# Kernel optimization log

Measured on AMD Instinct MI355X. Metric: run time of the kernel, lower is better.

Reference implementation:

```python
import jax, jax.numpy as jnp
import numpy as np

N, E = 50000, 800000
DN, DE, H = 128, 64, 8
C = DN // H  # per-head dim = 16


def setup_inputs() -> dict:
    key = jax.random.key(0)
    ks = jax.random.split(key, 16)
    s = 0.05
    inp = {
        "node_state": jax.random.normal(ks[0], (N, DN), jnp.float32),
        "edge_index": jax.random.randint(ks[1], (2, E), 0, N, jnp.int64 if jax.config.jax_enable_x64 else jnp.int32),
        "edge_state": jax.random.normal(ks[2], (E, DE), jnp.float32),
        # edge_proj: Linear(DE, DE)
        "W_edge": jax.random.normal(ks[3], (DE, DE), jnp.float32) * s,
        "b_edge": jnp.zeros((DE,), jnp.float32),
        # TransformerConv linears (in, out) layout: y = x @ W + b
        "Wq": jax.random.normal(ks[4], (DN, DN), jnp.float32) * s,
        "bq": jnp.zeros((DN,), jnp.float32),
        "Wk": jax.random.normal(ks[5], (DN, DN), jnp.float32) * s,
        "bk": jnp.zeros((DN,), jnp.float32),
        "Wv": jax.random.normal(ks[6], (DN, DN), jnp.float32) * s,
        "bv": jnp.zeros((DN,), jnp.float32),
        "We": jax.random.normal(ks[7], (DE, DN), jnp.float32) * s,  # lin_edge, no bias
        "Wskip": jax.random.normal(ks[8], (DN, DN), jnp.float32) * s,
        "bskip": jnp.zeros((DN,), jnp.float32),
        "Wbeta": jax.random.normal(ks[9], (3 * DN, 1), jnp.float32) * s,  # lin_beta, no bias
        "ln_g": jnp.ones((DN,), jnp.float32),
        "ln_b": jnp.zeros((DN,), jnp.float32),
    }
    return inp


def reference(node_state, edge_index, edge_state, W_edge, b_edge, Wq, bq, Wk, bk,
              Wv, bv, We, Wskip, bskip, Wbeta, ln_g, ln_b):
    n = node_state.shape[0]
    src, dst = edge_index[0], edge_index[1]

    # edge_proj
    edge_attr = edge_state @ W_edge + b_edge  # [E, DE]

    # TransformerConv (beta=True, concat=True, dropout in eval mode)
    q = (node_state @ Wq + bq).reshape(n, H, C)
    k = (node_state @ Wk + bk).reshape(n, H, C)
    v = (node_state @ Wv + bv).reshape(n, H, C)
    e = (edge_attr @ We).reshape(-1, H, C)  # [E, H, C]

    kj = k[src] + e                                        # [E, H, C]
    alpha = jnp.sum(q[dst] * kj, axis=-1) / np.sqrt(C)     # [E, H]

    # segment softmax over destination nodes
    amax = jax.ops.segment_max(alpha, dst, num_segments=n)  # [N, H]
    ex = jnp.exp(alpha - amax[dst])
    denom = jax.ops.segment_sum(ex, dst, num_segments=n)    # [N, H]
    a = ex / denom[dst]                                     # [E, H]

    msg = (v[src] + e) * a[:, :, None]                      # [E, H, C]
    out = jax.ops.segment_sum(msg, dst, num_segments=n).reshape(n, DN)

    # beta-gated skip
    x_r = node_state @ Wskip + bskip
    beta = jax.nn.sigmoid(jnp.concatenate([out, x_r, out - x_r], axis=-1) @ Wbeta)  # [N, 1]
    out = beta * x_r + (1.0 - beta) * out

    # LayerNorm
    mu = jnp.mean(out, axis=-1, keepdims=True)
    var = jnp.mean(jnp.square(out - mu), axis=-1, keepdims=True)
    normed = (out - mu) * jax.lax.rsqrt(var + 1e-5) * ln_g + ln_b

    # residual + relu (dropout is identity in eval)
    return node_state + jax.nn.relu(normed)
```

## Files before the change

kernel.cpp:

```cpp
#include <hip/hip_runtime.h>
#include <cstdint>
#include <cstddef>

#define NN 50000
#define NE 800000

typedef short bf16x8 __attribute__((ext_vector_type(8)));
typedef float f32x4 __attribute__((ext_vector_type(4)));
typedef float f32x2 __attribute__((ext_vector_type(2)));

__device__ __forceinline__ float b2f(unsigned short s) {
  union { unsigned int u; float f; } x; x.u = ((unsigned int)s) << 16; return x.f;
}
__device__ __forceinline__ unsigned short f2b(float f) {
  union { float f; unsigned int u; } x; x.f = f;
  unsigned int r = x.u + 0x7FFFu + ((x.u >> 16) & 1u);
  return (unsigned short)(r >> 16);
}

#define WS_WCE    0u
#define WS_BCE    16384u
#define WS_WCEF   20480u
#define WS_WALLF  40960u
#define WS_BALL   172032u
#define WS_QB     180224u
#define WS_KB     12980224u
#define WS_VB     25780224u
#define WS_XR     38580224u
#define WS_EB     64180224u
#define WS_CNT    268980224u
#define WS_OFF    269180224u
#define WS_CUR    269380224u
#define WS_BSUM   269580224u
#define WS_POS    269584320u
#define WS_SRCS   272784320u

__global__ void k_prep(const float* __restrict__ W_edge, const float* __restrict__ b_edge,
                       const float* __restrict__ We, unsigned short* __restrict__ wce,
                       float* __restrict__ bce) {
  int i = blockIdx.x;
  int j = threadIdx.x;
  float s = 0.f;
  for (int m = 0; m < 64; ++m) s += W_edge[i*64+m] * We[m*128+j];
  wce[i*128+j] = f2b(s);
  if (i == 0) {
    float bb = 0.f;
    for (int m = 0; m < 64; ++m) bb += b_edge[m] * We[m*128+j];
    bce[j] = bb;
  }
}

__global__ void k_pack_wce(const unsigned short* __restrict__ wce, unsigned short* __restrict__ wcef) {
  int fb = blockIdx.x;
  int ct = fb >> 1, s = fb & 1;
  int l = threadIdx.x;
  unsigned short* dst = wcef + (((size_t)(ct*2+s))*64 + l)*8;
  int col = ct*16 + (l & 15);
  int k0 = s*32 + (l >> 4)*8;
  #pragma unroll
  for (int j = 0; j < 8; ++j) dst[j] = wce[(k0+j)*128 + col];
}

__global__ void k_pack_wall(const float* __restrict__ Wq, const float* __restrict__ Wk,
                            const float* __restrict__ Wv, const float* __restrict__ Ws,
                            unsigned short* __restrict__ wallf) {
  int fb = blockIdx.x;
  int mat = fb >> 5, ct = (fb >> 2) & 7, s = fb & 3;
  int l = threadIdx.x;
  const float* W = (mat==0) ? Wq : (mat==1) ? Wk : (mat==2) ? Wv : Ws;
  unsigned short* dst = wallf + ((((size_t)(mat*8+ct))*4 + s)*64 + l)*8;
  int col = ct*16 + (l & 15);
  int k0 = s*32 + (l >> 4)*8;
  #pragma unroll
  for (int j = 0; j < 8; ++j) dst[j] = f2b(W[(k0+j)*128 + col]);
}

__global__ void k_pack_bias(const float* __restrict__ bq, const float* __restrict__ bk,
                            const float* __restrict__ bv, const float* __restrict__ bs,
                            float* __restrict__ ball) {
  int m = blockIdx.x, c = threadIdx.x;
  const float* b = (m==0) ? bq : (m==1) ? bk : (m==2) ? bv : bs;
  ball[m*128 + c] = b[c];
}

__global__ void __launch_bounds__(256) k_node_mfma(const float* __restrict__ x,
    const unsigned short* __restrict__ wallf, const float* __restrict__ ball,
    unsigned short* __restrict__ qb, unsigned short* __restrict__ kb,
    unsigned short* __restrict__ vb, float* __restrict__ xr) {
  __shared__ unsigned short sA[128*128];
  int mat = blockIdx.x & 3;
  int n0 = (blockIdx.x >> 2) * 128;
  for (int i = 0; i < 8; ++i) {
    int c = threadIdx.x + i*256;
    int row = c >> 4, ch = c & 15;
    int sw = (ch & 8) | ((ch & 7) ^ (row & 7));
    unsigned short tmp[8];
    if (n0 + row < NN) {
      const float* src = x + (size_t)(n0+row)*128 + ch*8;
      float4 f0 = *(const float4*)src;
      float4 f1 = *(const float4*)(src + 4);
      tmp[0]=f2b(f0.x); tmp[1]=f2b(f0.y); tmp[2]=f2b(f0.z); tmp[3]=f2b(f0.w);
      tmp[4]=f2b(f1.x); tmp[5]=f2b(f1.y); tmp[6]=f2b(f1.z); tmp[7]=f2b(f1.w);
    } else {
      #pragma unroll
      for (int j = 0; j < 8; ++j) tmp[j] = 0;
    }
    *(uint4*)&sA[row*128 + sw*8] = *(const uint4*)tmp;
  }
  __syncthreads();
  int l = threadIdx.x & 63, w = threadIdx.x >> 6;
  int g = l >> 4, ln = l & 15;
  f32x4 acc[2][8];
  #pragma unroll
  for (int rt = 0; rt < 2; ++rt)
    #pragma unroll
    for (int ct = 0; ct < 8; ++ct) acc[rt][ct] = (f32x4){0.f,0.f,0.f,0.f};
  for (int s = 0; s < 4; ++s) {
    bf16x8 wf[8];
    #pragma unroll
    for (int ct = 0; ct < 8; ++ct)
      wf[ct] = *(const bf16x8*)(wallf + ((((size_t)(mat*8+ct))*4 + s)*64 + l)*8);
    bf16x8 bfr[2];
    #pragma unroll
    for (int rt = 0; rt < 2; ++rt) {
      int row = w*32 + rt*16 + ln;
      int ch = s*4 + g;
      int sw = (ch & 8) | ((ch & 7) ^ (row & 7));
      bfr[rt] = *(const bf16x8*)&sA[row*128 + sw*8];
    }
    #pragma unroll
    for (int rt = 0; rt < 2; ++rt)
      #pragma unroll
      for (int ct = 0; ct < 8; ++ct)
        acc[rt][ct] = __builtin_amdgcn_mfma_f32_16x16x32_bf16(wf[ct], bfr[rt], acc[rt][ct], 0, 0, 0);
  }
  #pragma unroll
  for (int rt = 0; rt < 2; ++rt) {
    int node = n0 + w*32 + rt*16 + ln;
    if (node >= NN) continue;
    #pragma unroll
    for (int ct = 0; ct < 8; ++ct) {
      int c0 = ct*16 + g*4;
      float4 bi = *(const float4*)(ball + mat*128 + c0);
      float v0 = acc[rt][ct][0] + bi.x, v1 = acc[rt][ct][1] + bi.y;
      float v2 = acc[rt][ct][2] + bi.z, v3 = acc[rt][ct][3] + bi.w;
      if (mat == 3) {
        float4 o = {v0, v1, v2, v3};
        *(float4*)(xr + (size_t)node*128 + c0) = o;
      } else {
        unsigned short* dst = (mat==0) ? qb : (mat==1) ? kb : vb;
        unsigned short o[4] = {f2b(v0), f2b(v1), f2b(v2), f2b(v3)};
        *(uint2*)(dst + (size_t)node*128 + c0) = *(const uint2*)o;
      }
    }
  }
}

__global__ void __launch_bounds__(256) k_egemm_mfma(const float* __restrict__ es,
    const unsigned short* __restrict__ wcef, const float* __restrict__ bce,
    const int* __restrict__ pos, unsigned char* __restrict__ eb) {
  __shared__ unsigned short sA[128*64];
  __shared__ unsigned char  sO8[128*160];
  int e0 = blockIdx.x * 128;
  for (int i = 0; i < 4; ++i) {
    int c = threadIdx.x + i*256;
    int row = c >> 3, ch = c & 7;
    int sw = ch ^ (row & 7);
    const float* src = es + (size_t)(e0+row)*64 + ch*8;
    float4 f0 = *(const float4*)src;
    float4 f1 = *(const float4*)(src + 4);
    unsigned short tmp[8];
    tmp[0]=f2b(f0.x); tmp[1]=f2b(f0.y); tmp[2]=f2b(f0.z); tmp[3]=f2b(f0.w);
    tmp[4]=f2b(f1.x); tmp[5]=f2b(f1.y); tmp[6]=f2b(f1.z); tmp[7]=f2b(f1.w);
    *(uint4*)&sA[row*64 + sw*8] = *(const uint4*)tmp;
  }
  __syncthreads();
  int l = threadIdx.x & 63, w = threadIdx.x >> 6;
  int g = l >> 4, ln = l & 15;
  f32x4 acc[2][8];
  #pragma unroll
  for (int rt = 0; rt < 2; ++rt)
    #pragma unroll
    for (int ct = 0; ct < 8; ++ct) acc[rt][ct] = (f32x4){0.f,0.f,0.f,0.f};
  #pragma unroll
  for (int s = 0; s < 2; ++s) {
    bf16x8 wf[8];
    #pragma unroll
    for (int ct = 0; ct < 8; ++ct)
      wf[ct] = *(const bf16x8*)(wcef + (((size_t)(ct*2+s))*64 + l)*8);
    bf16x8 bfr[2];
    #pragma unroll
    for (int rt = 0; rt < 2; ++rt) {
      int row = w*32 + rt*16 + ln;
      int ch = (s*4 + g) ^ (row & 7);
      bfr[rt] = *(const bf16x8*)&sA[row*64 + ch*8];
    }
    #pragma unroll
    for (int rt = 0; rt < 2; ++rt)
      #pragma unroll
      for (int ct = 0; ct < 8; ++ct)
        acc[rt][ct] = __builtin_amdgcn_mfma_f32_16x16x32_bf16(wf[ct], bfr[rt], acc[rt][ct], 0, 0, 0);
  }
  #pragma unroll
  for (int rt = 0; rt < 2; ++rt) {
    int row = w*32 + rt*16 + ln;
    #pragma unroll
    for (int ct = 0; ct < 8; ++ct) {
      int c0 = ct*16 + g*4;
      float4 bi = *(const float4*)(bce + c0);
      int pk = 0;
      pk = __builtin_amdgcn_cvt_pk_fp8_f32(acc[rt][ct][0]+bi.x, acc[rt][ct][1]+bi.y, pk, false);
      pk = __builtin_amdgcn_cvt_pk_fp8_f32(acc[rt][ct][2]+bi.z, acc[rt][ct][3]+bi.w, pk, true);
      int ch = ct ^ (row & 7);
      *(int*)&sO8[row*160 + ch*16 + g*4] = pk;
    }
  }
  __syncthreads();
  int rrow = threadIdx.x >> 3;
  int rch  = threadIdx.x & 7;
  #pragma unroll
  for (int it = 0; it < 4; ++it) {
    int r = it*32 + rrow;
    int swc = rch ^ (r & 7);
    uint4 val = *(const uint4*)&sO8[r*160 + swc*16];
    int prow = pos[e0 + r];
    *(uint4*)(eb + (size_t)prow*128 + rch*16) = val;
  }
}

__global__ void __launch_bounds__(256) k_hist(const int* __restrict__ ei, int* __restrict__ cnt) {
  int t = blockIdx.x * 256 + threadIdx.x;
  if (t < NE) atomicAdd(&cnt[ei[NE + t]], 1);
}

__global__ void __launch_bounds__(256) k_scanA(const int* __restrict__ cnt,
    int* __restrict__ off, int* __restrict__ bsum) {
  __shared__ int s[256];
  int i = blockIdx.x * 256 + threadIdx.x;
  int v = (i < NN) ? cnt[i] : 0;
  s[threadIdx.x] = v;
  __syncthreads();
  #pragma unroll
  for (int d = 1; d < 256; d <<= 1) {
    int t = (threadIdx.x >= d) ? s[threadIdx.x - d] : 0;
    __syncthreads();
    s[threadIdx.x] += t;
    __syncthreads();
  }
  if (i < NN) off[i] = s[threadIdx.x] - v;
  if (threadIdx.x == 255) bsum[blockIdx.x] = s[255];
}

__global__ void __launch_bounds__(256) k_scanB(int* __restrict__ bsum, int nb) {
  __shared__ int s[256];
  int v = (threadIdx.x < nb) ? bsum[threadIdx.x] : 0;
  s[threadIdx.x] = v;
  __syncthreads();
  #pragma unroll
  for (int d = 1; d < 256; d <<= 1) {
    int t = (threadIdx.x >= d) ? s[threadIdx.x - d] : 0;
    __syncthreads();
    s[threadIdx.x] += t;
    __syncthreads();
  }
  if (threadIdx.x < nb) bsum[threadIdx.x] = s[threadIdx.x] - v;
}

__global__ void __launch_bounds__(256) k_scanC(int* __restrict__ off,
    const int* __restrict__ bsum, int* __restrict__ cur) {
  int i = blockIdx.x * 256 + threadIdx.x;
  if (i < NN) {
    int o = off[i] + bsum[blockIdx.x];
    off[i] = o;
    cur[i] = o;
  }
}

__global__ void __launch_bounds__(256) k_scatter(const int* __restrict__ ei,
    int* __restrict__ cur, int* __restrict__ pos, int* __restrict__ srcs) {
  int t = blockIdx.x * 256 + threadIdx.x;
  if (t < NE) {
    int d = ei[NE + t];
    int p = atomicAdd(&cur[d], 1);
    pos[t] = p;
    srcs[p] = ei[t];
  }
}

__global__ void __launch_bounds__(256) k_attn(
    const int* __restrict__ off, const int* __restrict__ cnt,
    const int* __restrict__ srcs,
    const unsigned short* __restrict__ qb, const unsigned short* __restrict__ kb,
    const unsigned short* __restrict__ vb, const unsigned char* __restrict__ eb,
    const float* __restrict__ xr, const float* __restrict__ x,
    const float* __restrict__ Wb, const float* __restrict__ ln_g,
    const float* __restrict__ ln_b, float* __restrict__ out) {
  int wid = threadIdx.x >> 6, lane = threadIdx.x & 63;
  int n = blockIdx.x * 4 + wid;
  if (n >= NN) return;
  int c = lane * 2;

  unsigned int qu = *(const unsigned int*)(qb + (size_t)n*128 + c);
  float q0 = b2f((unsigned short)(qu & 0xffffu)), q1 = b2f((unsigned short)(qu >> 16));

  int start = off[n], m = cnt[n];
  const int* sp = srcs + start;
  const unsigned char* ep = eb + (size_t)start*128 + c;
  float acc0 = 0.f, acc1 = 0.f, den = 0.f;

  auto body = [&](unsigned int ku, unsigned int eu16, unsigned int vu) {
    f32x2 ef = __builtin_amdgcn_cvt_pk_f32_fp8((int)eu16, false);
    float e0 = ef[0], e1 = ef[1];
    float p = q0*(b2f((unsigned short)(ku & 0xffffu)) + e0)
            + q1*(b2f((unsigned short)(ku >> 16)) + e1);
    p += __shfl_xor(p, 1);
    p += __shfl_xor(p, 2);
    p += __shfl_xor(p, 4);
    float a = __expf(p * 0.25f);
    den  += a;
    acc0 += a * (b2f((unsigned short)(vu & 0xffffu)) + e0);
    acc1 += a * (b2f((unsigned short)(vu >> 16)) + e1);
  };

  int i = 0;
  for (; i + 4 <= m; i += 4) {
    int sA = sp[i], sB = sp[i+1], sC = sp[i+2], sD = sp[i+3];
    unsigned int euA = *(const unsigned short*)(ep + (size_t)(i+0)*128);
    unsigned int euB = *(const unsigned short*)(ep + (size_t)(i+1)*128);
    unsigned int euC = *(const unsigned short*)(ep + (size_t)(i+2)*128);
    unsigned int euD = *(const unsigned short*)(ep + (size_t)(i+3)*128);
    unsigned int kuA = *(const unsigned int*)(kb + (size_t)sA*128 + c);
    unsigned int vuA = *(const unsigned int*)(vb + (size_t)sA*128 + c);
    unsigned int kuB = *(const unsigned int*)(kb + (size_t)sB*128 + c);
    unsigned int vuB = *(const unsigned int*)(vb + (size_t)sB*128 + c);
    unsigned int kuC = *(const unsigned int*)(kb + (size_t)sC*128 + c);
    unsigned int vuC = *(const unsigned int*)(vb + (size_t)sC*128 + c);
    unsigned int kuD = *(const unsigned int*)(kb + (size_t)sD*128 + c);
    unsigned int vuD = *(const unsigned int*)(vb + (size_t)sD*128 + c);
    body(kuA, euA, vuA);
    body(kuB, euB, vuB);
    body(kuC, euC, vuC);
    body(kuD, euD, vuD);
  }
  for (; i < m; ++i) {
    int sA = sp[i];
    unsigned int euA = *(const unsigned short*)(ep + (size_t)i*128);
    unsigned int kuA = *(const unsigned int*)(kb + (size_t)sA*128 + c);
    unsigned int vuA = *(const unsigned int*)(vb + (size_t)sA*128 + c);
    body(kuA, euA, vuA);
  }

  float inv = (m > 0) ? 1.f / den : 0.f;
  float o0 = acc0 * inv, o1 = acc1 * inv;

  float2 r = *(const float2*)(xr + (size_t)n*128 + c);
  float p = o0*Wb[c] + o1*Wb[c+1] + r.x*Wb[128+c] + r.y*Wb[128+c+1]
          + (o0-r.x)*Wb[256+c] + (o1-r.y)*Wb[256+c+1];
  #pragma unroll
  for (int offs = 32; offs > 0; offs >>= 1) p += __shfl_xor(p, offs);
  float beta = 1.f / (1.f + __expf(-p));
  float g0 = beta*r.x + (1.f-beta)*o0;
  float g1 = beta*r.y + (1.f-beta)*o1;
  float msum = g0 + g1;
  #pragma unroll
  for (int offs = 32; offs > 0; offs >>= 1) msum += __shfl_xor(msum, offs);
  msum *= (1.f/128.f);
  float d0 = g0 - msum, d1 = g1 - msum;
  float vv = d0*d0 + d1*d1;
  #pragma unroll
  for (int offs = 32; offs > 0; offs >>= 1) vv += __shfl_xor(vv, offs);
  vv *= (1.f/128.f);
  float rs = rsqrtf(vv + 1e-5f);
  float n0 = d0*rs*ln_g[c]   + ln_b[c];
  float n1 = d1*rs*ln_g[c+1] + ln_b[c+1];
  float2 xv = *(const float2*)(x + (size_t)n*128 + c);
  float2 res;
  res.x = xv.x + fmaxf(n0, 0.f);
  res.y = xv.y + fmaxf(n1, 0.f);
  *(float2*)(out + (size_t)n*128 + c) = res;
}

extern "C" void kernel_launch(void* const* d_in, const int* in_sizes, int n_in,
                              void* d_out, int out_size, void* d_ws, size_t ws_size,
                              hipStream_t stream) {
  const float* node   = (const float*)d_in[0];
  const int*   ei     = (const int*)  d_in[1];
  const float* es     = (const float*)d_in[2];
  const float* W_edge = (const float*)d_in[3];
  const float* b_edge = (const float*)d_in[4];
  const float* Wq     = (const float*)d_in[5];
  const float* bq     = (const float*)d_in[6];
  const float* Wk     = (const float*)d_in[7];
  const float* bk     = (const float*)d_in[8];
  const float* Wv     = (const float*)d_in[9];
  const float* bv     = (const float*)d_in[10];
  const float* We     = (const float*)d_in[11];
  const float* Wskip  = (const float*)d_in[12];
  const float* bskip  = (const float*)d_in[13];
  const float* Wbeta  = (const float*)d_in[14];
  const float* ln_g   = (const float*)d_in[15];
  const float* ln_b   = (const float*)d_in[16];

  char* ws = (char*)d_ws;
  unsigned short* wce   = (unsigned short*)(ws + WS_WCE);
  float*          bce   = (float*)(ws + WS_BCE);
  unsigned short* wcef  = (unsigned short*)(ws + WS_WCEF);
  unsigned short* wallf = (unsigned short*)(ws + WS_WALLF);
  float*          ball  = (float*)(ws + WS_BALL);
  unsigned short* qb  = (unsigned short*)(ws + WS_QB);
  unsigned short* kb  = (unsigned short*)(ws + WS_KB);
  unsigned short* vb  = (unsigned short*)(ws + WS_VB);
  float*          xr  = (float*)(ws + WS_XR);
  unsigned char*  eb  = (unsigned char*)(ws + WS_EB);
  int*            cnt = (int*)(ws + WS_CNT);
  int*            off = (int*)(ws + WS_OFF);
  int*            cur = (int*)(ws + WS_CUR);
  int*            bsm = (int*)(ws + WS_BSUM);
  int*            pos = (int*)(ws + WS_POS);
  int*            srcs= (int*)(ws + WS_SRCS);

  hipMemsetAsync(cnt, 0, (size_t)NN*4, stream);

  k_prep<<<64, 128, 0, stream>>>(W_edge, b_edge, We, wce, bce);
  k_pack_wce<<<16, 64, 0, stream>>>(wce, wcef);
  k_pack_wall<<<128, 64, 0, stream>>>(Wq, Wk, Wv, Wskip, wallf);
  k_pack_bias<<<4, 128, 0, stream>>>(bq, bk, bv, bskip, ball);

  const int nbScan = (NN + 255)/256;
  k_hist<<<(NE + 255)/256, 256, 0, stream>>>(ei, cnt);
  k_scanA<<<nbScan, 256, 0, stream>>>(cnt, off, bsm);
  k_scanB<<<1, 256, 0, stream>>>(bsm, nbScan);
  k_scanC<<<nbScan, 256, 0, stream>>>(off, bsm, cur);
  k_scatter<<<(NE + 255)/256, 256, 0, stream>>>(ei, cur, pos, srcs);

  const int ntiles = (NN + 127) / 128;
  k_node_mfma<<<ntiles*4, 256, 0, stream>>>(node, wallf, ball, qb, kb, vb, xr);
  k_egemm_mfma<<<NE/128, 256, 0, stream>>>(es, wcef, bce, pos, eb);

  k_attn<<<(NN + 3)/4, 256, 0, stream>>>(off, cnt, srcs, qb, kb, vb, eb,
                                         xr, node, Wbeta, ln_g, ln_b, (float*)d_out);
}
```

Before: 333.4 us.

## Merge node and edge GEMMs into one launch, store K/V as fp8

Result: faster. 284.4 us (-14.7%).

```diff
diff --git a/kernel.cpp b/kernel.cpp
--- a/kernel.cpp
+++ b/kernel.cpp
@@ -83,148 +83,133 @@
   ball[m*128 + c] = b[c];
 }
 
-__global__ void __launch_bounds__(256) k_node_mfma(const float* __restrict__ x,
-    const unsigned short* __restrict__ wallf, const float* __restrict__ ball,
-    unsigned short* __restrict__ qb, unsigned short* __restrict__ kb,
-    unsigned short* __restrict__ vb, float* __restrict__ xr) {
-  __shared__ unsigned short sA[128*128];
-  int mat = blockIdx.x & 3;
-  int n0 = (blockIdx.x >> 2) * 128;
-  for (int i = 0; i < 8; ++i) {
-    int c = threadIdx.x + i*256;
-    int row = c >> 4, ch = c & 15;
-    int sw = (ch & 8) | ((ch & 7) ^ (row & 7));
-    unsigned short tmp[8];
-    if (n0 + row < NN) {
-      const float* src = x + (size_t)(n0+row)*128 + ch*8;
-      float4 f0 = *(const float4*)src;
-      float4 f1 = *(const float4*)(src + 4);
-      tmp[0]=f2b(f0.x); tmp[1]=f2b(f0.y); tmp[2]=f2b(f0.z); tmp[3]=f2b(f0.w);
-      tmp[4]=f2b(f1.x); tmp[5]=f2b(f1.y); tmp[6]=f2b(f1.z); tmp[7]=f2b(f1.w);
-    } else {
-      #pragma unroll
-      for (int j = 0; j < 8; ++j) tmp[j] = 0;
-    }
-    *(uint4*)&sA[row*128 + sw*8] = *(const uint4*)tmp;
-  }
-  __syncthreads();
+__global__ void __launch_bounds__(256) k_mfma_all(
+    const float* __restrict__ x, const unsigned short* __restrict__ wallf,
+    const float* __restrict__ ball,
+    unsigned short* __restrict__ qb, unsigned char* __restrict__ kb,
+    unsigned char* __restrict__ vb, float* __restrict__ xr,
+    const float* __restrict__ es, const unsigned short* __restrict__ wcef,
+    const float* __restrict__ bce, const int* __restrict__ pos,
+    unsigned char* __restrict__ eb) {
+  __shared__ char smem[18432];
+  int b = blockIdx.x;
   int l = threadIdx.x & 63, w = threadIdx.x >> 6;
   int g = l >> 4, ln = l & 15;
-  f32x4 acc[2][8];
-  #pragma unroll
-  for (int rt = 0; rt < 2; ++rt)
-    #pragma unroll
-    for (int ct = 0; ct < 8; ++ct) acc[rt][ct] = (f32x4){0.f,0.f,0.f,0.f};
-  for (int s = 0; s < 4; ++s) {
-    bf16x8 wf[8];
-    #pragma unroll
-    for (int ct = 0; ct < 8; ++ct)
-      wf[ct] = *(const bf16x8*)(wallf + ((((size_t)(mat*8+ct))*4 + s)*64 + l)*8);
-    bf16x8 bfr[2];
-    #pragma unroll
-    for (int rt = 0; rt < 2; ++rt) {
-      int row = w*32 + rt*16 + ln;
+
+  if (b % 5 == 0) {
+    int tile = b / 5;
+    if (tile >= ((NN + 63)/64) * 4) return;
+    int mat = tile & 3;
+    int n0 = (tile >> 2) * 64;
+    unsigned short* sA = (unsigned short*)smem;
+    for (int i = 0; i < 4; ++i) {
+      int c = threadIdx.x + i*256;
+      int row = c >> 4, ch = c & 15;
+      int sw = (ch & 8) | ((ch & 7) ^ (row & 7));
+      unsigned short tmp[8];
+      if (n0 + row < NN) {
+        const float* src = x + (size_t)(n0+row)*128 + ch*8;
+        float4 f0 = *(const float4*)src;
+        float4 f1 = *(const float4*)(src + 4);
+        tmp[0]=f2b(f0.x); tmp[1]=f2b(f0.y); tmp[2]=f2b(f0.z); tmp[3]=f2b(f0.w);
+        tmp[4]=f2b(f1.x); tmp[5]=f2b(f1.y); tmp[6]=f2b(f1.z); tmp[7]=f2b(f1.w);
+      } else {
+        #pragma unroll
+        for (int j = 0; j < 8; ++j) tmp[j] = 0;
+      }
+      *(uint4*)&sA[row*128 + sw*8] = *(const uint4*)tmp;
+    }
+    __syncthreads();
+    f32x4 acc[8];
+    #pragma unroll
+    for (int ct = 0; ct < 8; ++ct) acc[ct] = (f32x4){0.f,0.f,0.f,0.f};
+    int row = w*16 + ln;
+    for (int s = 0; s < 4; ++s) {
       int ch = s*4 + g;
       int sw = (ch & 8) | ((ch & 7) ^ (row & 7));
-      bfr[rt] = *(const bf16x8*)&sA[row*128 + sw*8];
-    }
-    #pragma unroll
-    for (int rt = 0; rt < 2; ++rt)
+      bf16x8 bfr = *(const bf16x8*)&sA[row*128 + sw*8];
       #pragma unroll
-      for (int ct = 0; ct < 8; ++ct)
-        acc[rt][ct] = __builtin_amdgcn_mfma_f32_16x16x32_bf16(wf[ct], bfr[rt], acc[rt][ct], 0, 0, 0);
-  }
-  #pragma unroll
-  for (int rt = 0; rt < 2; ++rt) {
-    int node = n0 + w*32 + rt*16 + ln;
-    if (node >= NN) continue;
+      for (int ct = 0; ct < 8; ++ct) {
+        bf16x8 wf = *(const bf16x8*)(wallf + ((((size_t)(mat*8+ct))*4 + s)*64 + l)*8);
+        acc[ct] = __builtin_amdgcn_mfma_f32_16x16x32_bf16(wf, bfr, acc[ct], 0, 0, 0);
+      }
+    }
+    int node = n0 + row;
+    if (node >= NN) return;
     #pragma unroll
     for (int ct = 0; ct < 8; ++ct) {
       int c0 = ct*16 + g*4;
       float4 bi = *(const float4*)(ball + mat*128 + c0);
-      float v0 = acc[rt][ct][0] + bi.x, v1 = acc[rt][ct][1] + bi.y;
-      float v2 = acc[rt][ct][2] + bi.z, v3 = acc[rt][ct][3] + bi.w;
+      float v0 = acc[ct][0] + bi.x, v1 = acc[ct][1] + bi.y;
+      float v2 = acc[ct][2] + bi.z, v3 = acc[ct][3] + bi.w;
       if (mat == 3) {
         float4 o = {v0, v1, v2, v3};
         *(float4*)(xr + (size_t)node*128 + c0) = o;
+      } else if (mat == 0) {
+        unsigned short o[4] = {f2b(v0), f2b(v1), f2b(v2), f2b(v3)};
+        *(uint2*)(qb + (size_t)node*128 + c0) = *(const uint2*)o;
       } else {
-        unsigned short* dst = (mat==0) ? qb : (mat==1) ? kb : vb;
-        unsigned short o[4] = {f2b(v0), f2b(v1), f2b(v2), f2b(v3)};
-        *(uint2*)(dst + (size_t)node*128 + c0) = *(const uint2*)o;
+        int pk = 0;
+        pk = __builtin_amdgcn_cvt_pk_fp8_f32(v0, v1, pk, false);
+        pk = __builtin_amdgcn_cvt_pk_fp8_f32(v2, v3, pk, true);
+        unsigned char* dst = (mat==1) ? kb : vb;
+        *(int*)(dst + (size_t)node*128 + c0) = pk;
       }
     }
-  }
-}
-
-__global__ void __launch_bounds__(256) k_egemm_mfma(const float* __restrict__ es,
-    const unsigned short* __restrict__ wcef, const float* __restrict__ bce,
-    const int* __restrict__ pos, unsigned char* __restrict__ eb) {
-  __shared__ unsigned short sA[128*64];
-  __shared__ unsigned char  sO8[128*160];
-  int e0 = blockIdx.x * 128;
-  for (int i = 0; i < 4; ++i) {
-    int c = threadIdx.x + i*256;
-    int row = c >> 3, ch = c & 7;
-    int sw = ch ^ (row & 7);
-    const float* src = es + (size_t)(e0+row)*64 + ch*8;
-    float4 f0 = *(const float4*)src;
-    float4 f1 = *(const float4*)(src + 4);
-    unsigned short tmp[8];
-    tmp[0]=f2b(f0.x); tmp[1]=f2b(f0.y); tmp[2]=f2b(f0.z); tmp[3]=f2b(f0.w);
-    tmp[4]=f2b(f1.x); tmp[5]=f2b(f1.y); tmp[6]=f2b(f1.z); tmp[7]=f2b(f1.w);
-    *(uint4*)&sA[row*64 + sw*8] = *(const uint4*)tmp;
-  }
-  __syncthreads();
-  int l = threadIdx.x & 63, w = threadIdx.x >> 6;
-  int g = l >> 4, ln = l & 15;
-  f32x4 acc[2][8];
-  #pragma unroll
-  for (int rt = 0; rt < 2; ++rt)
-    #pragma unroll
-    for (int ct = 0; ct < 8; ++ct) acc[rt][ct] = (f32x4){0.f,0.f,0.f,0.f};
-  #pragma unroll
-  for (int s = 0; s < 2; ++s) {
-    bf16x8 wf[8];
-    #pragma unroll
-    for (int ct = 0; ct < 8; ++ct)
-      wf[ct] = *(const bf16x8*)(wcef + (((size_t)(ct*2+s))*64 + l)*8);
-    bf16x8 bfr[2];
-    #pragma unroll
-    for (int rt = 0; rt < 2; ++rt) {
-      int row = w*32 + rt*16 + ln;
+  } else {
+    int tile = b - b/5 - 1;
+    if (tile >= NE/64) return;
+    int e0 = tile * 64;
+    unsigned short* sA = (unsigned short*)smem;
+    unsigned char*  sO8 = (unsigned char*)(smem + 8192);
+    for (int i = 0; i < 2; ++i) {
+      int c = threadIdx.x + i*256;
+      int row = c >> 3, ch = c & 7;
+      int sw = ch ^ (row & 7);
+      const float* src = es + (size_t)(e0+row)*64 + ch*8;
+      float4 f0 = *(const float4*)src;
+      float4 f1 = *(const float4*)(src + 4);
+      unsigned short tmp[8];
+      tmp[0]=f2b(f0.x); tmp[1]=f2b(f0.y); tmp[2]=f2b(f0.z); tmp[3]=f2b(f0.w);
+      tmp[4]=f2b(f1.x); tmp[5]=f2b(f1.y); tmp[6]=f2b(f1.z); tmp[7]=f2b(f1.w);
+      *(uint4*)&sA[row*64 + sw*8] = *(const uint4*)tmp;
+    }
+    __syncthreads();
+    f32x4 acc[8];
+    #pragma unroll
+    for (int ct = 0; ct < 8; ++ct) acc[ct] = (f32x4){0.f,0.f,0.f,0.f};
+    int row = w*16 + ln;
+    #pragma unroll
+    for (int s = 0; s < 2; ++s) {
       int ch = (s*4 + g) ^ (row & 7);
-      bfr[rt] = *(const bf16x8*)&sA[row*64 + ch*8];
-    }
-    #pragma unroll
-    for (int rt = 0; rt < 2; ++rt)
+      bf16x8 bfr = *(const bf16x8*)&sA[row*64 + ch*8];
       #pragma unroll
-      for (int ct = 0; ct < 8; ++ct)
-        acc[rt][ct] = __builtin_amdgcn_mfma_f32_16x16x32_bf16(wf[ct], bfr[rt], acc[rt][ct], 0, 0, 0);
-  }
-  #pragma unroll
-  for (int rt = 0; rt < 2; ++rt) {
-    int row = w*32 + rt*16 + ln;
+      for (int ct = 0; ct < 8; ++ct) {
+        bf16x8 wf = *(const bf16x8*)(wcef + (((size_t)(ct*2+s))*64 + l)*8);
+        acc[ct] = __builtin_amdgcn_mfma_f32_16x16x32_bf16(wf, bfr, acc[ct], 0, 0, 0);
+      }
+    }
     #pragma unroll
     for (int ct = 0; ct < 8; ++ct) {
       int c0 = ct*16 + g*4;
       float4 bi = *(const float4*)(bce + c0);
       int pk = 0;
-      pk = __builtin_amdgcn_cvt_pk_fp8_f32(acc[rt][ct][0]+bi.x, acc[rt][ct][1]+bi.y, pk, false);
-      pk = __builtin_amdgcn_cvt_pk_fp8_f32(acc[rt][ct][2]+bi.z, acc[rt][ct][3]+bi.w, pk, true);
+      pk = __builtin_amdgcn_cvt_pk_fp8_f32(acc[ct][0]+bi.x, acc[ct][1]+bi.y, pk, false);
+      pk = __builtin_amdgcn_cvt_pk_fp8_f32(acc[ct][2]+bi.z, acc[ct][3]+bi.w, pk, true);
       int ch = ct ^ (row & 7);
       *(int*)&sO8[row*160 + ch*16 + g*4] = pk;
     }
-  }
-  __syncthreads();
-  int rrow = threadIdx.x >> 3;
-  int rch  = threadIdx.x & 7;
-  #pragma unroll
-  for (int it = 0; it < 4; ++it) {
-    int r = it*32 + rrow;
-    int swc = rch ^ (r & 7);
-    uint4 val = *(const uint4*)&sO8[r*160 + swc*16];
-    int prow = pos[e0 + r];
-    *(uint4*)(eb + (size_t)prow*128 + rch*16) = val;
+    __syncthreads();
+    int rrow = threadIdx.x >> 3;
+    int rch  = threadIdx.x & 7;
+    #pragma unroll
+    for (int it = 0; it < 2; ++it) {
+      int r = it*32 + rrow;
+      int swc = rch ^ (r & 7);
+      uint4 val = *(const uint4*)&sO8[r*160 + swc*16];
+      int prow = pos[e0 + r];
+      *(uint4*)(eb + (size_t)prow*128 + rch*16) = val;
+    }
   }
 }
 
@@ -290,8 +275,8 @@
 __global__ void __launch_bounds__(256) k_attn(
     const int* __restrict__ off, const int* __restrict__ cnt,
     const int* __restrict__ srcs,
-    const unsigned short* __restrict__ qb, const unsigned short* __restrict__ kb,
-    const unsigned short* __restrict__ vb, const unsigned char* __restrict__ eb,
+    const unsigned short* __restrict__ qb, const unsigned char* __restrict__ kb,
+    const unsigned char* __restrict__ vb, const unsigned char* __restrict__ eb,
     const float* __restrict__ xr, const float* __restrict__ x,
     const float* __restrict__ Wb, const float* __restrict__ ln_g,
     const float* __restrict__ ln_b, float* __restrict__ out) {
@@ -308,18 +293,18 @@
   const unsigned char* ep = eb + (size_t)start*128 + c;
   float acc0 = 0.f, acc1 = 0.f, den = 0.f;
 
-  auto body = [&](unsigned int ku, unsigned int eu16, unsigned int vu) {
-    f32x2 ef = __builtin_amdgcn_cvt_pk_f32_fp8((int)eu16, false);
-    float e0 = ef[0], e1 = ef[1];
-    float p = q0*(b2f((unsigned short)(ku & 0xffffu)) + e0)
-            + q1*(b2f((unsigned short)(ku >> 16)) + e1);
+  auto body = [&](unsigned int ku2, unsigned int eu2, unsigned int vu2) {
+    f32x2 ef = __builtin_amdgcn_cvt_pk_f32_fp8((int)eu2, false);
+    f32x2 kf = __builtin_amdgcn_cvt_pk_f32_fp8((int)ku2, false);
+    f32x2 vf = __builtin_amdgcn_cvt_pk_f32_fp8((int)vu2, false);
+    float p = q0*(kf[0] + ef[0]) + q1*(kf[1] + ef[1]);
     p += __shfl_xor(p, 1);
     p += __shfl_xor(p, 2);
     p += __shfl_xor(p, 4);
     float a = __expf(p * 0.25f);
     den  += a;
-    acc0 += a * (b2f((unsigned short)(vu & 0xffffu)) + e0);
-    acc1 += a * (b2f((unsigned short)(vu >> 16)) + e1);
+    acc0 += a * (vf[0] + ef[0]);
+    acc1 += a * (vf[1] + ef[1]);
   };
 
   int i = 0;
@@ -329,14 +314,14 @@
     unsigned int euB = *(const unsigned short*)(ep + (size_t)(i+1)*128);
     unsigned int euC = *(const unsigned short*)(ep + (size_t)(i+2)*128);
     unsigned int euD = *(const unsigned short*)(ep + (size_t)(i+3)*128);
-    unsigned int kuA = *(const unsigned int*)(kb + (size_t)sA*128 + c);
-    unsigned int vuA = *(const unsigned int*)(vb + (size_t)sA*128 + c);
-    unsigned int kuB = *(const unsigned int*)(kb + (size_t)sB*128 + c);
-    unsigned int vuB = *(const unsigned int*)(vb + (size_t)sB*128 + c);
-    unsigned int kuC = *(const unsigned int*)(kb + (size_t)sC*128 + c);
-    unsigned int vuC = *(const unsigned int*)(vb + (size_t)sC*128 + c);
-    unsigned int kuD = *(const unsigned int*)(kb + (size_t)sD*128 + c);
-    unsigned int vuD = *(const unsigned int*)(vb + (size_t)sD*128 + c);
+    unsigned int kuA = *(const unsigned short*)(kb + (size_t)sA*128 + c);
+    unsigned int vuA = *(const unsigned short*)(vb + (size_t)sA*128 + c);
+    unsigned int kuB = *(const unsigned short*)(kb + (size_t)sB*128 + c);
+    unsigned int vuB = *(const unsigned short*)(vb + (size_t)sB*128 + c);
+    unsigned int kuC = *(const unsigned short*)(kb + (size_t)sC*128 + c);
+    unsigned int vuC = *(const unsigned short*)(vb + (size_t)sC*128 + c);
+    unsigned int kuD = *(const unsigned short*)(kb + (size_t)sD*128 + c);
+    unsigned int vuD = *(const unsigned short*)(vb + (size_t)sD*128 + c);
     body(kuA, euA, vuA);
     body(kuB, euB, vuB);
     body(kuC, euC, vuC);
@@ -345,8 +330,8 @@
   for (; i < m; ++i) {
     int sA = sp[i];
     unsigned int euA = *(const unsigned short*)(ep + (size_t)i*128);
-    unsigned int kuA = *(const unsigned int*)(kb + (size_t)sA*128 + c);
-    unsigned int vuA = *(const unsigned int*)(vb + (size_t)sA*128 + c);
+    unsigned int kuA = *(const unsigned short*)(kb + (size_t)sA*128 + c);
+    unsigned int vuA = *(const unsigned short*)(vb + (size_t)sA*128 + c);
     body(kuA, euA, vuA);
   }
 
@@ -408,8 +393,8 @@
   unsigned short* wallf = (unsigned short*)(ws + WS_WALLF);
   float*          ball  = (float*)(ws + WS_BALL);
   unsigned short* qb  = (unsigned short*)(ws + WS_QB);
-  unsigned short* kb  = (unsigned short*)(ws + WS_KB);
-  unsigned short* vb  = (unsigned short*)(ws + WS_VB);
+  unsigned char*  kb  = (unsigned char*)(ws + WS_KB);
+  unsigned char*  vb  = (unsigned char*)(ws + WS_VB);
   float*          xr  = (float*)(ws + WS_XR);
   unsigned char*  eb  = (unsigned char*)(ws + WS_EB);
   int*            cnt = (int*)(ws + WS_CNT);
@@ -433,9 +418,10 @@
   k_scanC<<<nbScan, 256, 0, stream>>>(off, bsm, cur);
   k_scatter<<<(NE + 255)/256, 256, 0, stream>>>(ei, cur, pos, srcs);
 
-  const int ntiles = (NN + 127) / 128;
-  k_node_mfma<<<ntiles*4, 256, 0, stream>>>(node, wallf, ball, qb, kb, vb, xr);
-  k_egemm_mfma<<<NE/128, 256, 0, stream>>>(es, wcef, bce, pos, eb);
+  const int nodeTiles = ((NN + 63)/64) * 4;
+  const int grid = 5 * nodeTiles;
+  k_mfma_all<<<grid, 256, 0, stream>>>(node, wallf, ball, qb, kb, vb, xr,
+                                       es, wcef, bce, pos, eb);
 
   k_attn<<<(NN + 3)/4, 256, 0, stream>>>(off, cnt, srcs, qb, kb, vb, eb,
                                          xr, node, Wbeta, ln_g, ln_b, (float*)d_out);
```
